# Optimization experiments

Measured on AMD Instinct MI355X. Metric: run time of the kernel, lower is better.

## Reference

```python
import jax, jax.numpy as jnp
import numpy as np

N_CONST = 1.0
M_CONST = 11008.0

def setup_inputs() -> dict:
    key = jax.random.key(0)
    ks = jax.random.split(key, 7)
    N, LM_D, GNN_D, H = 131072, 1024, 200, 128
    lm_embeds = jax.random.normal(ks[0], (N, LM_D), dtype=jnp.float32)
    gnn_embeds = jax.random.normal(ks[1], (N, GNN_D), dtype=jnp.float32)
    neg_gnn_embeds = jax.random.normal(ks[2], (N, GNN_D), dtype=jnp.float32)
    lm_W = jax.random.normal(ks[3], (LM_D, H), dtype=jnp.float32) * (1.0 / np.sqrt(LM_D))
    lm_b = jnp.zeros((H,), dtype=jnp.float32)
    gnn_W = jax.random.normal(ks[4], (GNN_D, H), dtype=jnp.float32) * (1.0 / np.sqrt(GNN_D))
    gnn_b = jnp.zeros((H,), dtype=jnp.float32)
    return {"lm_embeds": lm_embeds, "gnn_embeds": gnn_embeds,
            "neg_gnn_embeds": neg_gnn_embeds,
            "lm_W": lm_W, "lm_b": lm_b, "gnn_W": gnn_W, "gnn_b": gnn_b}

def _l2norm(x):
    return x / jnp.linalg.norm(x, axis=-1, keepdims=True)

def _cal(lm_in, gnn_in, lm_W, lm_b, gnn_W, gnn_b, neg):
    l = _l2norm(lm_in @ lm_W + lm_b)       # [N, H]
    g = _l2norm(gnn_in @ gnn_W + gnn_b)    # [N, H]
    # diagonal of l @ g.T == per-row dot product (avoids NxN matmul)
    logits = jnp.exp(jnp.sum(l * g, axis=-1))  # [N]
    ratio = logits / (logits + N_CONST / M_CONST)
    return jnp.log(1.0 - ratio) if neg else jnp.log(ratio)

def reference(lm_embeds, gnn_embeds, neg_gnn_embeds, lm_W, lm_b, gnn_W, gnn_b):
    pos = jnp.mean(_cal(lm_embeds, gnn_embeds, lm_W, lm_b, gnn_W, gnn_b, False))
    neg = jnp.mean(_cal(lm_embeds, neg_gnn_embeds, lm_W, lm_b, gnn_W, gnn_b, True))
    return -pos - neg
```

## Files before the change

### kernel.cpp

```cpp
#include <hip/hip_runtime.h>
#include <hip/hip_bf16.h>
#include <stdint.h>

#define NROWS 131072
#define LMD   1024
#define GNND  200
#define HD    128
#define BLOCK 512
#define MTILE 128
#define NBLK  (NROWS/MTILE)
#define WCH   16384

typedef __attribute__((ext_vector_type(4))) float  f32x4;
typedef __attribute__((ext_vector_type(8))) short  bf16x8;

#define GLDS(SRC, DST) __builtin_amdgcn_global_load_lds( \
    (const __attribute__((address_space(1))) unsigned int*)(SRC), \
    (__attribute__((address_space(3))) unsigned int*)(DST), 16, 0, 0)
#define SCHED0  __builtin_amdgcn_sched_barrier(0)
#define BAR     __builtin_amdgcn_s_barrier()
#define VMW(N)  asm volatile("s_waitcnt vmcnt(" #N ")" ::: "memory")
#define LGKM0   asm volatile("s_waitcnt lgkmcnt(0)" ::: "memory")

__device__ __forceinline__ short f2bf(float x) {
    union { __hip_bfloat16 h; short s; } u;
    u.h = __float2bfloat16(x);
    return u.s;
}

__device__ __forceinline__ bf16x8 cvt8(f32x4 a, f32x4 b) {
    bf16x8 r;
    r[0]=f2bf(a[0]); r[1]=f2bf(a[1]); r[2]=f2bf(a[2]); r[3]=f2bf(a[3]);
    r[4]=f2bf(b[0]); r[5]=f2bf(b[1]); r[6]=f2bf(b[2]); r[7]=f2bf(b[3]);
    return r;
}

__device__ __forceinline__ float red16(float v) {
    #pragma unroll
    for (int m=1; m<16; m<<=1) v += __shfl_xor(v, m, 16);
    return v;
}

__global__ void prep_weights(const float* __restrict__ lm_W,
                             const float* __restrict__ gnn_W,
                             short* __restrict__ W1S, short* __restrict__ W2S)
{
    int idx = blockIdx.x*256 + threadIdx.x;
    int row = (idx >> 6) & 127;
    int e   = idx & 63;
    int kk  = (idx >> 13)*64 + (e ^ ((row & 7)*8));
    W1S[idx] = f2bf(lm_W[(long)kk*HD + row]);
    if (idx < 4*8192) {
        W2S[idx] = (kk < GNND) ? f2bf(gnn_W[(long)kk*HD + row]) : (short)0;
    }
}

__global__ __launch_bounds__(BLOCK) void fused(
    const float* __restrict__ lm,  const float* __restrict__ gnn,
    const float* __restrict__ ngn,
    const float* __restrict__ lm_b, const float* __restrict__ gnn_b,
    const char* __restrict__ W1S,  const char* __restrict__ W2S,
    float* __restrict__ partials)
{
    __shared__ short lbuf[4*8192];
    __shared__ float biasLDS[256];
    __shared__ float sp[8], sn[8];

    const int tid  = threadIdx.x;
    const int lane = tid & 63;
    const int win  = tid >> 6;
    const int col  = lane & 15;
    const int g    = lane >> 4;
    const int wq   = win*2048 + lane*16;
    const long row = (long)blockIdx.x * MTILE + win*16 + col;
    const int rotg = blockIdx.x & 7;

    const char* aL = (const char*)lm  + row*(LMD*4L)  + g*32;
    const char* aG = (const char*)gnn + row*(GNND*4L) + g*32;
    const char* aN = (const char*)ngn + row*(GNND*4L) + g*32;
    const char* clampG = (const char*)gnn + (size_t)NROWS*GNND*4 - 16;
    const char* clampN = (const char*)ngn + (size_t)NROWS*GNND*4 - 16;

    const float CC   = 1.0f / 11008.0f;
    const float LOGC = -9.3063777f;
    const f32x4 fz = {0.f,0.f,0.f,0.f};

    auto LOFF = [&](int p)->int { return ((p + rotg) & 7) * 512; };
    auto WSRC = [&](int p)->const char* {
        if (p < 16) {
            int lc = 2*(((p >> 1) + rotg) & 7) + (p & 1);
            return W1S + (size_t)lc*WCH;
        }
        return W2S + (size_t)(p - 16)*WCH;
    };

    auto ISSUEW = [&](const char* ws, int b) {
        const char* s = ws + wq;
        char* d = (char*)lbuf + (size_t)b*WCH + wq;
        #pragma unroll
        for (int i=0;i<2;i++) GLDS(s + i*1024, d + i*1024);
    };
    auto LOADG = [&](const char* base, int off, const char* cl, f32x4 (&S)[8]) {
        #pragma unroll
        for (int j=0;j<4;j++) {
            const char* p0 = base + off + j*128;
            const char* p1 = p0 + 16;
            if (cl) { if (p0 > cl) p0 = cl;  if (p1 > cl) p1 = cl; }
            S[2*j]   = *(const f32x4*)p0;
            S[2*j+1] = *(const f32x4*)p1;
        }
    };
    auto COMP = [&](int c, int half, f32x4 (&S)[8], f32x4 (&acc)[8]) {
        const short* wb = lbuf + (c & 3)*8192 + col*64;
        const int sw = (col & 7)*8;
        #pragma unroll
        for (int ks=0; ks<2; ++ks) {
            bf16x8 af = cvt8(S[half*4 + 2*ks], S[half*4 + 2*ks + 1]);
            const short* cb = wb + ((ks*32 + g*8) ^ sw);
            #pragma unroll
            for (int t=0;t<8;t++) {
                bf16x8 wf = *(const bf16x8*)(cb + t*1024);
                acc[t] = __builtin_amdgcn_mfma_f32_16x16x32_bf16(af, wf, acc[t], 0,0,0);
            }
        }
    };

    f32x4 accL[8], accG[8];
    #pragma unroll
    for (int t=0;t<8;t++) accL[t] = fz;
    f32x4 SA[8], SB[8];
    float pos_acc = 0.f, neg_acc = 0.f;

    if (tid < 256) {
        float bv = (tid < 128) ? lm_b[tid] : gnn_b[tid - 128];
        biasLDS[tid] = bv;
    }
    SCHED0;
    ISSUEW(WSRC(0), 0); ISSUEW(WSRC(1), 1); ISSUEW(WSRC(2), 2);
    LOADG(aL, LOFF(0), nullptr, SA);
    LOADG(aL, LOFF(1), nullptr, SB);
    SCHED0; VMW(20); LGKM0; SCHED0; BAR; SCHED0;

    #pragma unroll
    for (int gg=0; gg<8; ++gg) {
        f32x4 (&S)[8] = (gg & 1) ? SB : SA;
        ISSUEW(WSRC(2*gg+3), (2*gg+3) & 3);
        SCHED0;
        COMP(2*gg, 0, S, accL);
        SCHED0; VMW(12); SCHED0; BAR; SCHED0;
        ISSUEW(WSRC(2*gg+4), (2*gg+4) & 3);
        SCHED0;
        COMP(2*gg+1, 1, S, accL);
        SCHED0;
        if (gg < 6)       LOADG(aL, LOFF(gg+2), nullptr, S);
        else if (gg == 6) LOADG(aG,   0, clampG, S);
        else              LOADG(aG, 512, clampG, S);
        SCHED0; VMW(20); SCHED0; BAR; SCHED0;
    }

    #pragma unroll
    for (int t=0;t<8;t++) {
        float blv = biasLDS[t*16+col];
        #pragma unroll
        for (int r=0;r<4;r++) accL[t][r] += blv;
    }
    #pragma unroll
    for (int t=0;t<8;t++) accG[t] = fz;

    ISSUEW(WSRC(19), 3);
    SCHED0;
    COMP(16, 0, SA, accG);
    SCHED0; VMW(12); SCHED0; BAR; SCHED0;

    COMP(17, 1, SA, accG);
    SCHED0;
    LOADG(aN, 0, clampN, SA);
    SCHED0; VMW(18); SCHED0; BAR; SCHED0;

    COMP(18, 0, SB, accG);
    SCHED0; VMW(8); SCHED0; BAR; SCHED0;

    COMP(19, 1, SB, accG);
    SCHED0;
    LOADG(aN, 512, clampN, SB);
    SCHED0;

    #pragma unroll
    for (int r=0;r<4;r++) {
        float lg=0.f, ll=0.f, gg2=0.f;
        #pragma unroll
        for (int t=0;t<8;t++) {
            float lv=accL[t][r], gv=accG[t][r] + biasLDS[128+t*16+col];
            lg += lv*gv; ll += lv*lv; gg2 += gv*gv;
        }
        lg=red16(lg); ll=red16(ll); gg2=red16(gg2);
        float d  = lg * rsqrtf(ll*gg2);
        float pi = d - logf(expf(d)+CC);
        if (col==0) pos_acc += pi;
    }
    #pragma unroll
    for (int t=0;t<8;t++) accG[t] = fz;

    COMP(20, 0, SA, accG);
    COMP(21, 1, SA, accG);
    COMP(22, 0, SB, accG);
    COMP(23, 1, SB, accG);

    #pragma unroll
    for (int r=0;r<4;r++) {
        float ln=0.f, nn=0.f, ll=0.f;
        #pragma unroll
        for (int t=0;t<8;t++) {
            float lv=accL[t][r], nv=accG[t][r] + biasLDS[128+t*16+col];
            ln += lv*nv; nn += nv*nv; ll += lv*lv;
        }
        ln=red16(ln); nn=red16(nn); ll=red16(ll);
        float d  = ln * rsqrtf(ll*nn);
        float ni = LOGC - logf(expf(d)+CC);
        if (col==0) neg_acc += ni;
    }

    #pragma unroll
    for (int m=1;m<64;m<<=1) {
        pos_acc += __shfl_xor(pos_acc, m, 64);
        neg_acc += __shfl_xor(neg_acc, m, 64);
    }
    if (lane==0) { sp[win]=pos_acc; sn[win]=neg_acc; }
    __syncthreads();
    if (tid==0) {
        float p=0.f,n=0.f;
        #pragma unroll
        for (int w=0;w<8;w++){ p+=sp[w]; n+=sn[w]; }
        partials[blockIdx.x*2]   = p;
        partials[blockIdx.x*2+1] = n;
    }
}

__global__ void finalize(const float* __restrict__ partials, float* __restrict__ out)
{
    __shared__ float sp[256], sn[256];
    float p=0.f, n=0.f;
    for (int i=threadIdx.x; i<NBLK; i+=256) { p += partials[2*i]; n += partials[2*i+1]; }
    sp[threadIdx.x]=p; sn[threadIdx.x]=n;
    __syncthreads();
    for (int s=128; s>0; s>>=1) {
        if ((int)threadIdx.x < s) { sp[threadIdx.x]+=sp[threadIdx.x+s]; sn[threadIdx.x]+=sn[threadIdx.x+s]; }
        __syncthreads();
    }
    if (threadIdx.x==0) out[0] = -(sp[0]+sn[0]) / (float)NROWS;
}

extern "C" void kernel_launch(void* const* d_in, const int* in_sizes, int n_in,
                              void* d_out, int out_size, void* d_ws, size_t ws_size,
                              hipStream_t stream)
{
    const float* lm    = (const float*)d_in[0];
    const float* gnn   = (const float*)d_in[1];
    const float* ngn   = (const float*)d_in[2];
    const float* lm_W  = (const float*)d_in[3];
    const float* lm_b  = (const float*)d_in[4];
    const float* gnn_W = (const float*)d_in[5];
    const float* gnn_b = (const float*)d_in[6];

    short* W1S = (short*)d_ws;
    short* W2S = (short*)((char*)d_ws + 262144);
    float* partials = (float*)((char*)d_ws + 262144 + 65536);

    prep_weights<<<512, 256, 0, stream>>>(lm_W, gnn_W, W1S, W2S);
    fused<<<NBLK, BLOCK, 0, stream>>>(lm, gnn, ngn, lm_b, gnn_b,
                                      (const char*)W1S, (const char*)W2S, partials);
    finalize<<<1, 256, 0, stream>>>(partials, (float*)d_out);
}
```

Before: 169.6 us.

## Restructure weight-chunk pipeline to double-buffer pairs with one barrier per step

The weight-streaming pipeline moves from a 4-slot ring with one chunk prefetched per half-step (two barriers per step) to a pairwise double buffer. Two chunks are issued together into the idle pair of slots, then both halves are computed from the other pair. This halves the number of workgroup barriers and waitcnt points in the main loop and in the gnn phase, cutting sync stalls. In exchange the prefetch distance per chunk shrinks and loads arrive in bursts, which may expose more memory latency.

Result: faster. 163.1 us (-3.8%).

```diff
diff --git a/kernel.cpp b/kernel.cpp
--- a/kernel.cpp
+++ b/kernel.cpp
@@ -86,12 +86,12 @@
     const f32x4 fz = {0.f,0.f,0.f,0.f};
 
     auto LOFF = [&](int p)->int { return ((p + rotg) & 7) * 512; };
-    auto WSRC = [&](int p)->const char* {
-        if (p < 16) {
-            int lc = 2*(((p >> 1) + rotg) & 7) + (p & 1);
+    auto WSRC = [&](int c)->const char* {
+        if (c < 16) {
+            int lc = 2*(((c >> 1) + rotg) & 7) + (c & 1);
             return W1S + (size_t)lc*WCH;
         }
-        return W2S + (size_t)(p - 16)*WCH;
+        return W2S + (size_t)(c - 16)*WCH;
     };
 
     auto ISSUEW = [&](const char* ws, int b) {
@@ -110,8 +110,8 @@
             S[2*j+1] = *(const f32x4*)p1;
         }
     };
-    auto COMP = [&](int c, int half, f32x4 (&S)[8], f32x4 (&acc)[8]) {
-        const short* wb = lbuf + (c & 3)*8192 + col*64;
+    auto COMP = [&](int b, int half, f32x4 (&S)[8], f32x4 (&acc)[8]) {
+        const short* wb = lbuf + b*8192 + col*64;
         const int sw = (col & 7)*8;
         #pragma unroll
         for (int ks=0; ks<2; ++ks) {
@@ -136,26 +136,26 @@
         biasLDS[tid] = bv;
     }
     SCHED0;
-    ISSUEW(WSRC(0), 0); ISSUEW(WSRC(1), 1); ISSUEW(WSRC(2), 2);
+    ISSUEW(WSRC(0), 0); ISSUEW(WSRC(1), 1);
     LOADG(aL, LOFF(0), nullptr, SA);
     LOADG(aL, LOFF(1), nullptr, SB);
-    SCHED0; VMW(20); LGKM0; SCHED0; BAR; SCHED0;
-
-    #pragma unroll
-    for (int gg=0; gg<8; ++gg) {
-        f32x4 (&S)[8] = (gg & 1) ? SB : SA;
-        ISSUEW(WSRC(2*gg+3), (2*gg+3) & 3);
+    SCHED0; VMW(16); LGKM0; SCHED0; BAR; SCHED0;
+
+    #pragma unroll
+    for (int s = 0; s < 8; ++s) {
+        f32x4 (&S)[8] = (s & 1) ? SB : SA;
+        const int rp = 2*(s & 1);
+        const int wp = 2*((s+1) & 1);
+        ISSUEW(WSRC(2*s+2), wp);
+        ISSUEW(WSRC(2*s+3), wp+1);
         SCHED0;
-        COMP(2*gg, 0, S, accL);
-        SCHED0; VMW(12); SCHED0; BAR; SCHED0;
-        ISSUEW(WSRC(2*gg+4), (2*gg+4) & 3);
+        COMP(rp,   0, S, accL);
+        COMP(rp+1, 1, S, accL);
         SCHED0;
-        COMP(2*gg+1, 1, S, accL);
-        SCHED0;
-        if (gg < 6)       LOADG(aL, LOFF(gg+2), nullptr, S);
-        else if (gg == 6) LOADG(aG,   0, clampG, S);
-        else              LOADG(aG, 512, clampG, S);
-        SCHED0; VMW(20); SCHED0; BAR; SCHED0;
+        if (s < 6)       LOADG(aL, LOFF(s+2), nullptr, S);
+        else if (s == 6) LOADG(aG,   0, clampG, S);
+        else             LOADG(aG, 512, clampG, S);
+        SCHED0; VMW(8); SCHED0; BAR; SCHED0;
     }
 
     #pragma unroll
@@ -167,20 +167,17 @@
     #pragma unroll
     for (int t=0;t<8;t++) accG[t] = fz;
 
+    ISSUEW(WSRC(18), 2);
     ISSUEW(WSRC(19), 3);
     SCHED0;
-    COMP(16, 0, SA, accG);
-    SCHED0; VMW(12); SCHED0; BAR; SCHED0;
-
-    COMP(17, 1, SA, accG);
+    COMP(0, 0, SA, accG);
+    COMP(1, 1, SA, accG);
     SCHED0;
     LOADG(aN, 0, clampN, SA);
-    SCHED0; VMW(18); SCHED0; BAR; SCHED0;
-
-    COMP(18, 0, SB, accG);
     SCHED0; VMW(8); SCHED0; BAR; SCHED0;
 
-    COMP(19, 1, SB, accG);
+    COMP(2, 0, SB, accG);
+    COMP(3, 1, SB, accG);
     SCHED0;
     LOADG(aN, 512, clampN, SB);
     SCHED0;
@@ -201,10 +198,10 @@
     #pragma unroll
     for (int t=0;t<8;t++) accG[t] = fz;
 
-    COMP(20, 0, SA, accG);
-    COMP(21, 1, SA, accG);
-    COMP(22, 0, SB, accG);
-    COMP(23, 1, SB, accG);
+    COMP(0, 0, SA, accG);
+    COMP(1, 1, SA, accG);
+    COMP(2, 0, SB, accG);
+    COMP(3, 1, SB, accG);
 
     #pragma unroll
     for (int r=0;r<4;r++) {
```
